# Kernel optimization log

Hardware: AMD Instinct MI355X
Metric: run time of the kernel (lower is better)

## Reference

```python
import jax, jax.numpy as jnp
from jax import lax
import numpy as np

B, N, E, F = 32, 256, 8, 16
NEIGH = 31            # neighbourhood_size
K1 = NEIGH + 1        # subgraph size = neigh_size + 1


def setup_inputs() -> dict:
    rng = np.random.default_rng(0)
    # Connected symmetric adjacency: backbone chain + random extra pairs (no self loops).
    A = np.zeros((B, N, N), np.float32)
    i = np.arange(N - 1)
    A[:, i, i + 1] = 1.0
    A[:, i + 1, i] = 1.0
    for b in range(B):
        pairs = rng.integers(0, N, size=(N, 2))
        pairs = pairs[pairs[:, 0] != pairs[:, 1]]
        A[b, pairs[:, 0], pairs[:, 1]] = 1.0
        A[b, pairs[:, 1], pairs[:, 0]] = 1.0
    A[:, np.arange(N), np.arange(N)] = 0.0
    key = jax.random.key(0)
    k1, k2 = jax.random.split(key)
    edges = jax.random.normal(k1, (B, N, N, E), dtype=jnp.float32)
    feats = jax.random.normal(k2, (B, N, F), dtype=jnp.float32)
    return {"adj_batch": jnp.asarray(A), "edges_batch": edges, "features_batch": feats}


def _bfs(adj_bool, start):
    """Ordered BFS from `start`, collecting K1 vertices (matches get_neighbours:
    FIFO queue, neighbours enqueued in ascending index order, dedup vs seen)."""
    n = adj_bool.shape[0]
    queue = jnp.zeros((n + 1,), jnp.int32).at[0].set(start)  # slot n is a dummy sink
    seen = jnp.zeros((n,), bool).at[start].set(True)
    processed = jnp.zeros((K1,), jnp.int32)

    def body(i, st):
        queue, seen, head, tail, processed = st
        cur = queue[head]
        processed = processed.at[i].set(cur)
        nbr = adj_bool[cur] & ~seen                      # new frontier, index order
        cum = jnp.cumsum(nbr.astype(jnp.int32))
        pos = jnp.where(nbr, tail + cum - 1, n)          # compacted queue slots
        queue = queue.at[pos].set(jnp.arange(n, dtype=jnp.int32))
        return queue, seen | nbr, head + 1, tail + cum[-1], processed

    st = lax.fori_loop(0, K1, body, (queue, seen, jnp.int32(0), jnp.int32(1), processed))
    return st[4]  # [K1] BFS ordering


def reference(adj_batch, edges_batch, features_batch):
    adj_bool = adj_batch != 0
    starts = jnp.arange(adj_batch.shape[1], dtype=jnp.int32)
    # proc: [B, N, K1] local->original vertex mapping per (graph, centre vertex)
    proc = jax.vmap(lambda ab: jax.vmap(lambda s: _bfs(ab, s))(starts))(adj_bool)

    def gather(adj, edges, feats, p):
        pi = p[:, :, None]                               # [N, K1, 1]
        pj = p[:, None, :]                               # [N, 1, K1]
        sub_adj = adj[pi, pj]                            # [N, K1, K1]
        mask = (sub_adj != 0)[..., None]
        sub_edges = jnp.where(mask, edges[pi, pj], 0.0)  # [N, K1, K1, E]
        sub_feats = feats[p]                             # [N, K1, F]
        return sub_adj, sub_edges, sub_feats

    return jax.vmap(gather)(adj_batch, edges_batch, features_batch, proc)
```

## Files before the change

### kernel.cpp

```cpp
#include <hip/hip_runtime.h>
#include <stdint.h>

#define Bb 32
#define Nn 256
#define Ee 8
#define Ff 16
#define K1 32

typedef unsigned long long u64;

__global__ void bitmask_kernel(const float* __restrict__ adj, u64* __restrict__ bm) {
    int wave = (blockIdx.x << 2) + (threadIdx.x >> 6);
    int lane = threadIdx.x & 63;
    const float* row = adj + (size_t)wave * Nn;
#pragma unroll
    for (int w = 0; w < 4; ++w) {
        float v = row[w * 64 + lane];
        u64 m = __ballot(v != 0.0f);
        if (lane == 0) bm[(size_t)wave * 4 + w] = m;
    }
}

__global__ void bfs_kernel(const u64* __restrict__ bm, uint32_t* __restrict__ proc32) {
    __shared__ u64 bml[Nn * 4];
    __shared__ uint8_t order[Nn * K1];
    int b = blockIdx.x;
    int t = threadIdx.x;
#pragma unroll
    for (int k = 0; k < 4; ++k) bml[t + k * 256] = bm[(size_t)b * 1024 + t + k * 256];
    uint32_t* ord32 = (uint32_t*)order;
#pragma unroll
    for (int k = 0; k < 8; ++k) ord32[t + k * 256] = 0;
    __syncthreads();

    int s = t;
    u64 seen[4];
#pragma unroll
    for (int w = 0; w < 4; ++w) seen[w] = (w == (s >> 6)) ? (1ull << (s & 63)) : 0ull;
    order[s * K1] = (uint8_t)s;
    int count = 1;
    for (int i = 0; i < count && count < K1; ++i) {
        int cur = order[s * K1 + i];
#pragma unroll
        for (int w = 0; w < 4; ++w) {
            u64 nw = bml[cur * 4 + w] & ~seen[w];
            seen[w] |= nw;
            while (nw) {
                int bit = __builtin_ctzll(nw);
                nw &= nw - 1;
                if (count < K1) order[s * K1 + count++] = (uint8_t)(w * 64 + bit);
                else break;
            }
        }
    }
    __syncthreads();
#pragma unroll
    for (int k = 0; k < 8; ++k) proc32[(size_t)b * 2048 + t + k * 256] = ord32[t + k * 256];
}

__global__ void gather_kernel(const float4* __restrict__ e4,
                              const float4* __restrict__ feats4,
                              const u64* __restrict__ bm,
                              const uint32_t* __restrict__ proc32,
                              float* __restrict__ out) {
    int bs = blockIdx.x;
    int b = bs >> 8;
    int t = threadIdx.x;
    __shared__ int p[K1];
    __shared__ u64 bmrow[K1][4];

    if (t < 8) {
        uint32_t w = proc32[(size_t)bs * 8 + t];
        p[t * 4 + 0] = w & 255;
        p[t * 4 + 1] = (w >> 8) & 255;
        p[t * 4 + 2] = (w >> 16) & 255;
        p[t * 4 + 3] = (w >> 24) & 255;
    }
    __syncthreads();
    if (t < 128) {
        int i = t >> 2, w = t & 3;
        bmrow[i][w] = bm[((size_t)b * 256 + p[i]) * 4 + w];
    }
    __syncthreads();

    float4* out0 = (float4*)(out) + (size_t)bs * 256;
    {
        int i = t >> 3;
        int j0 = (t & 7) * 4;
        float4 a;
        int pj;
        pj = p[j0 + 0]; a.x = (float)((bmrow[i][pj >> 6] >> (pj & 63)) & 1ull);
        pj = p[j0 + 1]; a.y = (float)((bmrow[i][pj >> 6] >> (pj & 63)) & 1ull);
        pj = p[j0 + 2]; a.z = (float)((bmrow[i][pj >> 6] >> (pj & 63)) & 1ull);
        pj = p[j0 + 3]; a.w = (float)((bmrow[i][pj >> 6] >> (pj & 63)) & 1ull);
        out0[t] = a;
    }

    float4* out2 = (float4*)(out + 75497472ull) + (size_t)bs * 128;
    if (t < 128) {
        int i = t >> 2, f4 = t & 3;
        out2[t] = feats4[((size_t)b * 256 + p[i]) * 4 + f4];
    }

    float4* out1 = (float4*)(out + 8388608ull) + (size_t)bs * 2048;
#pragma unroll
    for (int k = 0; k < 8; ++k) {
        int v = t + k * 256;
        int i = v >> 6, j = (v >> 1) & 31, h = v & 1;
        int pi = p[i], pj = p[j];
        bool m = (bmrow[i][pj >> 6] >> (pj & 63)) & 1ull;
        float4 val = make_float4(0.f, 0.f, 0.f, 0.f);
        if (m) val = e4[(((size_t)b * 256 + pi) * 256 + pj) * 2 + h];
        out1[v] = val;
    }
}

extern "C" void kernel_launch(void* const* d_in, const int* in_sizes, int n_in,
                              void* d_out, int out_size, void* d_ws, size_t ws_size,
                              hipStream_t stream) {
    const float* adj   = (const float*)d_in[0];
    const float* edges = (const float*)d_in[1];
    const float* feats = (const float*)d_in[2];
    float* out = (float*)d_out;

    u64* bm = (u64*)d_ws;
    uint32_t* proc32 = (uint32_t*)((char*)d_ws + (size_t)Bb * Nn * 4 * sizeof(u64));

    bitmask_kernel<<<Bb * Nn / 4, 256, 0, stream>>>(adj, bm);
    bfs_kernel<<<Bb, 256, 0, stream>>>(bm, proc32);
    gather_kernel<<<Bb * Nn, 256, 0, stream>>>((const float4*)edges, (const float4*)feats,
                                               bm, proc32, out);
}
```

Measured before the change: 87.28 us.

## Split BFS across more blocks and use nontemporal stores in gather

The BFS kernel now launches four 64-thread blocks per graph instead of one 256-thread block, each handling 64 start vertices. This spreads the serial, divergent BFS over more compute units and drops the zero-init of the order buffer. The gather kernel writes its outputs with nontemporal stores through a vector type, to keep the large streaming writes from polluting the cache. The cost is that each of the four BFS blocks reloads the whole adjacency bitmask into shared memory.

```diff
diff --git a/kernel.cpp b/kernel.cpp
--- a/kernel.cpp
+++ b/kernel.cpp
@@ -8,6 +8,7 @@
 #define K1 32
 
 typedef unsigned long long u64;
+typedef float f32x4 __attribute__((ext_vector_type(4)));
 
 __global__ void bitmask_kernel(const float* __restrict__ adj, u64* __restrict__ bm) {
     int wave = (blockIdx.x << 2) + (threadIdx.x >> 6);
@@ -23,24 +24,22 @@
 
 __global__ void bfs_kernel(const u64* __restrict__ bm, uint32_t* __restrict__ proc32) {
     __shared__ u64 bml[Nn * 4];
-    __shared__ uint8_t order[Nn * K1];
-    int b = blockIdx.x;
+    __shared__ uint8_t order[64 * K1];
+    int b = blockIdx.x >> 2;
+    int g = blockIdx.x & 3;
     int t = threadIdx.x;
 #pragma unroll
-    for (int k = 0; k < 4; ++k) bml[t + k * 256] = bm[(size_t)b * 1024 + t + k * 256];
-    uint32_t* ord32 = (uint32_t*)order;
-#pragma unroll
-    for (int k = 0; k < 8; ++k) ord32[t + k * 256] = 0;
+    for (int k = 0; k < 16; ++k) bml[t + k * 64] = bm[(size_t)b * 1024 + t + k * 64];
     __syncthreads();
 
-    int s = t;
+    int s = g * 64 + t;
     u64 seen[4];
 #pragma unroll
     for (int w = 0; w < 4; ++w) seen[w] = (w == (s >> 6)) ? (1ull << (s & 63)) : 0ull;
-    order[s * K1] = (uint8_t)s;
+    order[t * K1] = (uint8_t)s;
     int count = 1;
     for (int i = 0; i < count && count < K1; ++i) {
-        int cur = order[s * K1 + i];
+        int cur = order[t * K1 + i];
 #pragma unroll
         for (int w = 0; w < 4; ++w) {
             u64 nw = bml[cur * 4 + w] & ~seen[w];
@@ -48,18 +47,20 @@
             while (nw) {
                 int bit = __builtin_ctzll(nw);
                 nw &= nw - 1;
-                if (count < K1) order[s * K1 + count++] = (uint8_t)(w * 64 + bit);
+                if (count < K1) order[t * K1 + count++] = (uint8_t)(w * 64 + bit);
                 else break;
             }
         }
     }
     __syncthreads();
+    const uint32_t* ord32 = (const uint32_t*)order;
 #pragma unroll
-    for (int k = 0; k < 8; ++k) proc32[(size_t)b * 2048 + t + k * 256] = ord32[t + k * 256];
+    for (int k = 0; k < 8; ++k)
+        proc32[(size_t)b * 2048 + g * 512 + t + k * 64] = ord32[t + k * 64];
 }
 
-__global__ void gather_kernel(const float4* __restrict__ e4,
-                              const float4* __restrict__ feats4,
+__global__ void gather_kernel(const f32x4* __restrict__ e4,
+                              const f32x4* __restrict__ feats4,
                               const u64* __restrict__ bm,
                               const uint32_t* __restrict__ proc32,
                               float* __restrict__ out) {
@@ -83,35 +84,36 @@
     }
     __syncthreads();
 
-    float4* out0 = (float4*)(out) + (size_t)bs * 256;
+    f32x4* out0 = (f32x4*)(out) + (size_t)bs * 256;
     {
         int i = t >> 3;
         int j0 = (t & 7) * 4;
-        float4 a;
+        f32x4 a;
         int pj;
         pj = p[j0 + 0]; a.x = (float)((bmrow[i][pj >> 6] >> (pj & 63)) & 1ull);
         pj = p[j0 + 1]; a.y = (float)((bmrow[i][pj >> 6] >> (pj & 63)) & 1ull);
         pj = p[j0 + 2]; a.z = (float)((bmrow[i][pj >> 6] >> (pj & 63)) & 1ull);
         pj = p[j0 + 3]; a.w = (float)((bmrow[i][pj >> 6] >> (pj & 63)) & 1ull);
-        out0[t] = a;
+        __builtin_nontemporal_store(a, out0 + t);
     }
 
-    float4* out2 = (float4*)(out + 75497472ull) + (size_t)bs * 128;
+    f32x4* out2 = (f32x4*)(out + 75497472ull) + (size_t)bs * 128;
     if (t < 128) {
         int i = t >> 2, f4 = t & 3;
-        out2[t] = feats4[((size_t)b * 256 + p[i]) * 4 + f4];
+        f32x4 v = feats4[((size_t)b * 256 + p[i]) * 4 + f4];
+        __builtin_nontemporal_store(v, out2 + t);
     }
 
-    float4* out1 = (float4*)(out + 8388608ull) + (size_t)bs * 2048;
+    f32x4* out1 = (f32x4*)(out + 8388608ull) + (size_t)bs * 2048;
 #pragma unroll
     for (int k = 0; k < 8; ++k) {
         int v = t + k * 256;
         int i = v >> 6, j = (v >> 1) & 31, h = v & 1;
         int pi = p[i], pj = p[j];
         bool m = (bmrow[i][pj >> 6] >> (pj & 63)) & 1ull;
-        float4 val = make_float4(0.f, 0.f, 0.f, 0.f);
+        f32x4 val = (f32x4){0.f, 0.f, 0.f, 0.f};
         if (m) val = e4[(((size_t)b * 256 + pi) * 256 + pj) * 2 + h];
-        out1[v] = val;
+        __builtin_nontemporal_store(val, out1 + v);
     }
 }
 
@@ -127,7 +129,7 @@
     uint32_t* proc32 = (uint32_t*)((char*)d_ws + (size_t)Bb * Nn * 4 * sizeof(u64));
 
     bitmask_kernel<<<Bb * Nn / 4, 256, 0, stream>>>(adj, bm);
-    bfs_kernel<<<Bb, 256, 0, stream>>>(bm, proc32);
-    gather_kernel<<<Bb * Nn, 256, 0, stream>>>((const float4*)edges, (const float4*)feats,
+    bfs_kernel<<<Bb * 4, 64, 0, stream>>>(bm, proc32);
+    gather_kernel<<<Bb * Nn, 256, 0, stream>>>((const f32x4*)edges, (const f32x4*)feats,
                                                bm, proc32, out);
 }
```

After: 91.89 us. 1.05x slower.
